# Kernel tuning notes

Hardware: AMD Instinct MI355X
Metric: run time of the kernel (lower is better)

Reference implementation:

```python
import jax, jax.numpy as jnp
import numpy as np

B = 256      # batch size
N = 8192     # neurons per layer (uniform layer width)
E = 262144   # edges per layer (avg in-degree 32)
L = 4        # number of edge layers


def setup_inputs() -> dict:
    key = jax.random.key(0)
    k_x, k_src, k_dst, k_w = jax.random.split(key, 4)
    x = jax.random.normal(k_x, (B, N), dtype=jnp.float32)
    edge_src = jax.random.randint(k_src, (L, E), 0, N)  # source neuron in prev layer
    edge_dst = jax.random.randint(k_dst, (L, E), 0, N)  # dest neuron in curr layer
    # torch init: randn(num_edges) * sqrt(2 / (prev_size + curr_size))
    w_scale = float(np.sqrt(2.0 / (N + N)))
    weights = jax.random.normal(k_w, (L, E), dtype=jnp.float32) * w_scale
    bias = jnp.zeros((L, N), dtype=jnp.float32)  # torch.zeros init
    return {"x": x, "weights": weights, "bias": bias,
            "edge_src": edge_src, "edge_dst": edge_dst}


def reference(x, weights, bias, edge_src, edge_dst):
    """Per layer: gather(src) * w -> scatter_add(dst) -> + bias -> relu."""
    out = x  # [B, N]
    for l in range(L):  # small fixed number of structurally distinct layers
        src = edge_src[l]          # [E]
        dst = edge_dst[l]          # [E]
        gathered = out[:, src] * weights[l]  # [B, E] weighted source activations
        # scatter_add over destination neurons (duplicates accumulate)
        agg = jax.ops.segment_sum(gathered.T, dst, num_segments=N).T  # [B, N]
        out = jax.nn.relu(agg + bias[l])
    return out
```

## Files before the change

kernel.cpp:

```cpp
#include <hip/hip_runtime.h>


static constexpr int BATCH = 256;
static constexpr int NN    = 8192;
static constexpr int NE    = 262144;
static constexpr int NL    = 4;
static constexpr int NBUK  = 128;
static constexpr int BCAP  = 3072;
static constexpr int CHUNK = 2048;

__device__ inline unsigned bf16rne(float f) {
  unsigned u = __float_as_uint(f);
  return (u + 0x7fffu + ((u >> 16) & 1u)) >> 16;
}
__device__ inline float bf16tof(unsigned us) { return __uint_as_float(us << 16); }
__device__ inline float blo(unsigned u) { return __uint_as_float(u << 16); }
__device__ inline float bhi(unsigned u) { return __uint_as_float(u & 0xffff0000u); }

__global__ void transpose_in_k(const float* __restrict__ in, ushort* __restrict__ out) {
  __shared__ float tile[32][33];
  int c0 = blockIdx.x * 32, r0 = blockIdx.y * 32;
  int tx = threadIdx.x, ty = threadIdx.y;
#pragma unroll
  for (int i = ty; i < 32; i += 8)
    tile[i][tx] = in[(size_t)(r0 + i) * NN + (c0 + tx)];
  __syncthreads();
#pragma unroll
  for (int i = ty; i < 32; i += 8)
    out[(size_t)(c0 + i) * BATCH + (r0 + tx)] = (ushort)bf16rne(tile[tx][i]);
}

__global__ void transpose_out_k(const ushort* __restrict__ in, float* __restrict__ out) {
  __shared__ float tile[32][33];
  int c0 = blockIdx.x * 32, r0 = blockIdx.y * 32;
  int tx = threadIdx.x, ty = threadIdx.y;
#pragma unroll
  for (int i = ty; i < 32; i += 8)
    tile[i][tx] = bf16tof(in[(size_t)(r0 + i) * BATCH + (c0 + tx)]);
  __syncthreads();
#pragma unroll
  for (int i = ty; i < 32; i += 8)
    out[(size_t)(c0 + i) * NN + (r0 + tx)] = tile[tx][i];
}

__global__ void zero_k(int* __restrict__ p) { p[threadIdx.x] = 0; }

__global__ void part_k(const int* __restrict__ src, const int* __restrict__ dst,
                       const float* __restrict__ w, int* __restrict__ bcur,
                       uint2* __restrict__ stag) {
  __shared__ int cnt[NBUK], sc[NBUK], loff[NBUK], gbase[NBUK], lcur[NBUK];
  __shared__ uint2 ebuf[CHUNK];
  __shared__ unsigned char bkt[CHUNK];
  int t = threadIdx.x;
  int l = blockIdx.x >> 7;
  size_t e0 = (size_t)blockIdx.x * CHUNK;
  if (t < NBUK) cnt[t] = 0;
  __syncthreads();
  int es[8], ed[8]; float ew[8];
#pragma unroll
  for (int k = 0; k < 8; ++k) {
    size_t e = e0 + t + k * 256;
    es[k] = src[e]; ed[k] = dst[e]; ew[k] = w[e];
    atomicAdd(&cnt[ed[k] >> 6], 1);
  }
  __syncthreads();
  if (t < NBUK) sc[t] = cnt[t];
  __syncthreads();
  for (int off = 1; off < NBUK; off <<= 1) {
    int v = 0;
    if (t < NBUK && t >= off) v = sc[t - off];
    __syncthreads();
    if (t < NBUK) sc[t] += v;
    __syncthreads();
  }
  if (t < NBUK) {
    int excl = sc[t] - cnt[t];
    loff[t] = excl;
    lcur[t] = excl;
    gbase[t] = atomicAdd(&bcur[(l << 7) + t], cnt[t]);
  }
  __syncthreads();
#pragma unroll
  for (int k = 0; k < 8; ++k) {
    int b = ed[k] >> 6;
    int p = atomicAdd(&lcur[b], 1);
    ebuf[p] = make_uint2((unsigned)es[k] | ((unsigned)(ed[k] & 63) << 16),
                         __float_as_uint(ew[k]));
    bkt[p]  = (unsigned char)b;
  }
  __syncthreads();
#pragma unroll
  for (int k = 0; k < 8; ++k) {
    int i = t + k * 256;
    int b = bkt[i];
    int gp = gbase[b] + (i - loff[b]);
    if (gp < BCAP)
      stag[(size_t)((l << 7) + b) * BCAP + gp] = ebuf[i];
  }
}

__global__ void place_k(const uint2* __restrict__ stag, const int* __restrict__ bcur,
                        float2* __restrict__ csr, int* __restrict__ rp) {
  __shared__ int bc[NBUK], bsc[NBUK];
  __shared__ int cnt[64], sc64[64], lcur[64];
  __shared__ uint2 ebuf[BCAP];
  int t = threadIdx.x;
  int gb = blockIdx.x, l = gb >> 7, b = gb & 127;
  if (t < NBUK) { bc[t] = min(bcur[(l << 7) + t], BCAP); bsc[t] = bc[t]; }
  if (t < 64) cnt[t] = 0;
  __syncthreads();
  for (int off = 1; off < NBUK; off <<= 1) {
    int v = 0;
    if (t < NBUK && t >= off) v = bsc[t - off];
    __syncthreads();
    if (t < NBUK) bsc[t] += v;
    __syncthreads();
  }
  int n   = bc[b];
  int seg = bsc[b] - bc[b];
  for (int i = t; i < n; i += 256)
    ebuf[i] = stag[(size_t)gb * BCAP + i];
  __syncthreads();
  for (int i = t; i < n; i += 256)
    atomicAdd(&cnt[(ebuf[i].x >> 16) & 63], 1);
  __syncthreads();
  if (t < 64) sc64[t] = cnt[t];
  __syncthreads();
  for (int off = 1; off < 64; off <<= 1) {
    int v = 0;
    if (t < 64 && t >= off) v = sc64[t - off];
    __syncthreads();
    if (t < 64) sc64[t] += v;
    __syncthreads();
  }
  if (t < 64) {
    int excl = sc64[t] - cnt[t];
    lcur[t] = excl;
    rp[l * (NN + 1) + (b << 6) + t] = seg + excl;
  }
  if (b == 127 && t == 65) rp[l * (NN + 1) + NN] = bsc[127];
  __syncthreads();
  for (int i = t; i < n; i += 256) {
    uint2 r = ebuf[i];
    int p = atomicAdd(&lcur[(r.x >> 16) & 63], 1);
    csr[(size_t)l * NE + seg + p] =
        make_float2(__int_as_float((int)(r.x & 0xffffu)), __uint_as_float(r.y));
  }
}

__global__ void gather_k(const ushort* __restrict__ act, ushort* __restrict__ out,
                         const float2* __restrict__ csr, const int* __restrict__ rp,
                         const float* __restrict__ bias) {
  int row  = blockIdx.x * 4 + (threadIdx.x >> 6);
  int lane = threadIdx.x & 63;
  int half = lane >> 5;
  int l32  = lane & 31;
  int k0 = rp[row], k1 = rp[row + 1];
  float4 accA = make_float4(0.f, 0.f, 0.f, 0.f);
  float4 accB = make_float4(0.f, 0.f, 0.f, 0.f);
  const ushort* actc = act + l32 * 8;
  for (int kc = k0; kc < k1; kc += 64) {
    int nk = k1 - kc;
    if (nk > 64) nk = 64;
    int ksel = lane < nk ? lane : nk - 1;
    unsigned long long mu =
        __builtin_nontemporal_load((const unsigned long long*)(csr + kc + ksel));
    int sv = (int)(mu & 0xffffffffu);
    int wv = (int)(mu >> 32);
    int npair = (nk + 1) >> 1;
#pragma unroll 8
    for (int j = 0; j < npair; ++j) {
      int  idx   = 2 * j + half;
      bool valid = idx < nk;
      int  qi    = valid ? idx : 0;
      int   s  = __shfl(sv, qi);
      float wt = __int_as_float(__shfl(wv, qi));
      wt = valid ? wt : 0.f;
      uint4 v = *(const uint4*)(actc + (size_t)s * BATCH);
      accA.x += wt * blo(v.x); accA.y += wt * bhi(v.x);
      accA.z += wt * blo(v.y); accA.w += wt * bhi(v.y);
      accB.x += wt * blo(v.z); accB.y += wt * bhi(v.z);
      accB.z += wt * blo(v.w); accB.w += wt * bhi(v.w);
    }
  }
  accA.x += __shfl(accA.x, lane ^ 32); accA.y += __shfl(accA.y, lane ^ 32);
  accA.z += __shfl(accA.z, lane ^ 32); accA.w += __shfl(accA.w, lane ^ 32);
  accB.x += __shfl(accB.x, lane ^ 32); accB.y += __shfl(accB.y, lane ^ 32);
  accB.z += __shfl(accB.z, lane ^ 32); accB.w += __shfl(accB.w, lane ^ 32);
  if (half == 0) {
    float b = bias[row];
    uint4 o;
    o.x = bf16rne(fmaxf(accA.x + b, 0.f)) | (bf16rne(fmaxf(accA.y + b, 0.f)) << 16);
    o.y = bf16rne(fmaxf(accA.z + b, 0.f)) | (bf16rne(fmaxf(accA.w + b, 0.f)) << 16);
    o.z = bf16rne(fmaxf(accB.x + b, 0.f)) | (bf16rne(fmaxf(accB.y + b, 0.f)) << 16);
    o.w = bf16rne(fmaxf(accB.z + b, 0.f)) | (bf16rne(fmaxf(accB.w + b, 0.f)) << 16);
    *(uint4*)(out + (size_t)row * BATCH + l32 * 8) = o;
  }
}

extern "C" void kernel_launch(void* const* d_in, const int* in_sizes, int n_in,
                              void* d_out, int out_size, void* d_ws, size_t ws_size,
                              hipStream_t stream) {
  const float* x       = (const float*)d_in[0];
  const float* weights = (const float*)d_in[1];
  const float* bias    = (const float*)d_in[2];
  const int*   esrc    = (const int*)d_in[3];
  const int*   edst    = (const int*)d_in[4];
  float*       out     = (float*)d_out;

  char* p = (char*)d_ws;
  float2* csr     = (float2*)p; p += (size_t)NL * NE * 8;
  int*    row_ptr = (int*)p;    p += (size_t)NL * (NN + 1) * 4;
  int*    bcur    = (int*)p;    p += (size_t)NL * NBUK * 4;
  uint2*  stag    = (uint2*)p;
  ushort* actA    = (ushort*)p;
  ushort* actB    = actA + (size_t)NN * BATCH;

  zero_k<<<1, NL * NBUK, 0, stream>>>(bcur);
  part_k<<<(NL * NE) / CHUNK, 256, 0, stream>>>(esrc, edst, weights, bcur, stag);
  place_k<<<NL * NBUK, 256, 0, stream>>>(stag, bcur, csr, row_ptr);

  transpose_in_k<<<dim3(NN / 32, BATCH / 32), dim3(32, 8), 0, stream>>>(x, actA);

  for (int l = 0; l < NL; ++l) {
    gather_k<<<NN / 4, 256, 0, stream>>>(actA, actB,
                                         csr + (size_t)l * NE,
                                         row_ptr + (size_t)l * (NN + 1),
                                         bias + (size_t)l * NN);
    ushort* t = actA; actA = actB; actB = t;
  }

  transpose_out_k<<<dim3(BATCH / 32, NN / 32), dim3(32, 8), 0, stream>>>(actA, out);
}
```

Before: 100.8 us.

## Split gather batch dimension into four slices with eight edges per wavefront step

The gather kernel now splits the 256-wide batch into four 64-column slices, each handled by its own block, so the grid grows fourfold. Within a wavefront, 8 lanes cover one slice row (128 bytes) and 8 edges are processed at once instead of 2, followed by a three-level xor-shuffle reduction. This raises memory-level parallelism per wavefront and the total number of wavefronts in flight. The cost is that CSR edges and row pointers are read four times per layer and each gathered row read shrinks to 128 bytes.

New measurement: 133.7 us. 32.6% more time.

```diff
diff --git a/kernel.cpp b/kernel.cpp
--- a/kernel.cpp
+++ b/kernel.cpp
@@ -148,17 +148,20 @@
   }
 }
 
-__global__ void gather_k(const ushort* __restrict__ act, ushort* __restrict__ out,
-                         const float2* __restrict__ csr, const int* __restrict__ rp,
-                         const float* __restrict__ bias) {
-  int row  = blockIdx.x * 4 + (threadIdx.x >> 6);
+__global__ __launch_bounds__(256) void
+gather_k(const ushort* __restrict__ act, ushort* __restrict__ out,
+         const float2* __restrict__ csr, const int* __restrict__ rp,
+         const float* __restrict__ bias) {
+  int slice = blockIdx.x >> 11;
+  int rowblk = blockIdx.x & 2047;
+  int row  = rowblk * 4 + (threadIdx.x >> 6);
   int lane = threadIdx.x & 63;
-  int half = lane >> 5;
-  int l32  = lane & 31;
+  int slot = lane >> 3;
+  int cp   = lane & 7;
   int k0 = rp[row], k1 = rp[row + 1];
-  float4 accA = make_float4(0.f, 0.f, 0.f, 0.f);
-  float4 accB = make_float4(0.f, 0.f, 0.f, 0.f);
-  const ushort* actc = act + l32 * 8;
+  float4 a0 = make_float4(0.f, 0.f, 0.f, 0.f);
+  float4 a1 = make_float4(0.f, 0.f, 0.f, 0.f);
+  const ushort* actc = act + slice * 64 + cp * 8;
   for (int kc = k0; kc < k1; kc += 64) {
     int nk = k1 - kc;
     if (nk > 64) nk = 64;
@@ -167,34 +170,38 @@
         __builtin_nontemporal_load((const unsigned long long*)(csr + kc + ksel));
     int sv = (int)(mu & 0xffffffffu);
     int wv = (int)(mu >> 32);
-    int npair = (nk + 1) >> 1;
-#pragma unroll 8
-    for (int j = 0; j < npair; ++j) {
-      int  idx   = 2 * j + half;
+    int niter = (nk + 7) >> 3;
+#pragma unroll 4
+    for (int j = 0; j < niter; ++j) {
+      int  idx   = 8 * j + slot;
       bool valid = idx < nk;
       int  qi    = valid ? idx : 0;
       int   s  = __shfl(sv, qi);
       float wt = __int_as_float(__shfl(wv, qi));
       wt = valid ? wt : 0.f;
       uint4 v = *(const uint4*)(actc + (size_t)s * BATCH);
-      accA.x += wt * blo(v.x); accA.y += wt * bhi(v.x);
-      accA.z += wt * blo(v.y); accA.w += wt * bhi(v.y);
-      accB.x += wt * blo(v.z); accB.y += wt * bhi(v.z);
-      accB.z += wt * blo(v.w); accB.w += wt * bhi(v.w);
+      a0.x += wt * blo(v.x); a0.y += wt * bhi(v.x);
+      a0.z += wt * blo(v.y); a0.w += wt * bhi(v.y);
+      a1.x += wt * blo(v.z); a1.y += wt * bhi(v.z);
+      a1.z += wt * blo(v.w); a1.w += wt * bhi(v.w);
     }
   }
-  accA.x += __shfl(accA.x, lane ^ 32); accA.y += __shfl(accA.y, lane ^ 32);
-  accA.z += __shfl(accA.z, lane ^ 32); accA.w += __shfl(accA.w, lane ^ 32);
-  accB.x += __shfl(accB.x, lane ^ 32); accB.y += __shfl(accB.y, lane ^ 32);
-  accB.z += __shfl(accB.z, lane ^ 32); accB.w += __shfl(accB.w, lane ^ 32);
-  if (half == 0) {
+  a0.x += __shfl_xor(a0.x, 8); a0.x += __shfl_xor(a0.x, 16); a0.x += __shfl_xor(a0.x, 32);
+  a0.y += __shfl_xor(a0.y, 8); a0.y += __shfl_xor(a0.y, 16); a0.y += __shfl_xor(a0.y, 32);
+  a0.z += __shfl_xor(a0.z, 8); a0.z += __shfl_xor(a0.z, 16); a0.z += __shfl_xor(a0.z, 32);
+  a0.w += __shfl_xor(a0.w, 8); a0.w += __shfl_xor(a0.w, 16); a0.w += __shfl_xor(a0.w, 32);
+  a1.x += __shfl_xor(a1.x, 8); a1.x += __shfl_xor(a1.x, 16); a1.x += __shfl_xor(a1.x, 32);
+  a1.y += __shfl_xor(a1.y, 8); a1.y += __shfl_xor(a1.y, 16); a1.y += __shfl_xor(a1.y, 32);
+  a1.z += __shfl_xor(a1.z, 8); a1.z += __shfl_xor(a1.z, 16); a1.z += __shfl_xor(a1.z, 32);
+  a1.w += __shfl_xor(a1.w, 8); a1.w += __shfl_xor(a1.w, 16); a1.w += __shfl_xor(a1.w, 32);
+  if (slot == 0) {
     float b = bias[row];
     uint4 o;
-    o.x = bf16rne(fmaxf(accA.x + b, 0.f)) | (bf16rne(fmaxf(accA.y + b, 0.f)) << 16);
-    o.y = bf16rne(fmaxf(accA.z + b, 0.f)) | (bf16rne(fmaxf(accA.w + b, 0.f)) << 16);
-    o.z = bf16rne(fmaxf(accB.x + b, 0.f)) | (bf16rne(fmaxf(accB.y + b, 0.f)) << 16);
-    o.w = bf16rne(fmaxf(accB.z + b, 0.f)) | (bf16rne(fmaxf(accB.w + b, 0.f)) << 16);
-    *(uint4*)(out + (size_t)row * BATCH + l32 * 8) = o;
+    o.x = bf16rne(fmaxf(a0.x + b, 0.f)) | (bf16rne(fmaxf(a0.y + b, 0.f)) << 16);
+    o.y = bf16rne(fmaxf(a0.z + b, 0.f)) | (bf16rne(fmaxf(a0.w + b, 0.f)) << 16);
+    o.z = bf16rne(fmaxf(a1.x + b, 0.f)) | (bf16rne(fmaxf(a1.y + b, 0.f)) << 16);
+    o.w = bf16rne(fmaxf(a1.z + b, 0.f)) | (bf16rne(fmaxf(a1.w + b, 0.f)) << 16);
+    *(uint4*)(out + (size_t)row * BATCH + slice * 64 + cp * 8) = o;
   }
 }
 
@@ -223,10 +230,10 @@
   transpose_in_k<<<dim3(NN / 32, BATCH / 32), dim3(32, 8), 0, stream>>>(x, actA);
 
   for (int l = 0; l < NL; ++l) {
-    gather_k<<<NN / 4, 256, 0, stream>>>(actA, actB,
-                                         csr + (size_t)l * NE,
-                                         row_ptr + (size_t)l * (NN + 1),
-                                         bias + (size_t)l * NN);
+    gather_k<<<(NN / 4) * 4, 256, 0, stream>>>(actA, actB,
+                                               csr + (size_t)l * NE,
+                                               row_ptr + (size_t)l * (NN + 1),
+                                               bias + (size_t)l * NN);
     ushort* t = actA; actA = actB; actB = t;
   }
 
```
